# Performance work log

Measured on AMD Instinct MI355X. Metric: run time of the kernel, lower is better.

## Reference

```python
import jax, jax.numpy as jnp
import numpy as np

B, S, D = 4, 2048, 1024
H, DK, DV = 16, 64, 64  # heads, key_size, size_per_head
NEG = 1000000000.0


def setup_inputs() -> dict:
    key = jax.random.key(0)
    ks = jax.random.split(key, 8)
    scale = 1.0 / np.sqrt(D)
    return {
        "q": jax.random.normal(ks[0], (B, S, D), jnp.float32),
        "k": jax.random.normal(ks[1], (B, S, D), jnp.float32),
        "v": jax.random.normal(ks[2], (B, S, D), jnp.float32),
        "v_mask": jax.random.randint(ks[3], (B, S), 0, 2).astype(jnp.float32),
        "q_mask": jax.random.randint(ks[4], (B, S), 0, 2).astype(jnp.float32),
        "Wq": jax.random.normal(ks[5], (D, H * DK), jnp.float32) * scale,
        "Wk": jax.random.normal(ks[6], (D, H * DK), jnp.float32) * scale,
        "Wv": jax.random.normal(ks[7], (D, H * DV), jnp.float32) * scale,
    }


def reference(q, k, v, v_mask, q_mask, Wq, Wk, Wv):
    b, sq, _ = q.shape
    sk = k.shape[1]
    # projections + head split: [B, H, S, Dh]
    qw = (q @ Wq).reshape(b, sq, H, DK).transpose(0, 2, 1, 3)
    kw = (k @ Wk).reshape(b, sk, H, DK).transpose(0, 2, 1, 3)
    vw = (v @ Wv).reshape(b, sk, H, DV).transpose(0, 2, 1, 3)
    # scaled dot-product scores [B, H, Sq, Sk]
    a = jnp.einsum("bhqd,bhkd->bhqk", qw, kw) / jnp.sqrt(jnp.float32(DK))
    # additive kv-mask (v_mask over key axis)
    a = a - (1.0 - v_mask)[:, None, None, :] * NEG
    # causal (mask_right=True): subtract 1e9 on strictly-upper triangle
    causal = jnp.triu(jnp.ones((sq, sk), jnp.float32), k=1) * NEG
    a = a - causal[None, None]
    a = jax.nn.softmax(a, axis=-1)
    o = jnp.einsum("bhqk,bhkd->bhqd", a, vw)
    o = o.transpose(0, 2, 1, 3).reshape(b, sq, H * DV)
    # multiplicative query mask on output
    return o * q_mask[:, :, None]
```

## Files before the change

### kernel.cpp

```cpp
#include <hip/hip_runtime.h>

#define S_LEN 2048
#define NHEAD 16

typedef float f32x4 __attribute__((ext_vector_type(4)));
typedef __bf16 bf16x8 __attribute__((ext_vector_type(8)));
typedef __bf16 bf16x4 __attribute__((ext_vector_type(4)));

#define AS1 __attribute__((address_space(1)))
#define AS3 __attribute__((address_space(3)))

__device__ __forceinline__ void gl2lds16(const void* g, void* l) {
    __builtin_amdgcn_global_load_lds((const AS1 unsigned int*)g,
                                     (AS3 unsigned int*)l, 16, 0, 0);
}
__device__ __forceinline__ void wb_leave4() {
    asm volatile("s_waitcnt vmcnt(4)\n\ts_barrier" ::: "memory");
}
__device__ __forceinline__ void wb_drain() {
    asm volatile("s_waitcnt vmcnt(0)\n\ts_barrier" ::: "memory");
}

__global__ __launch_bounds__(256) void cast_swizzle_kernel(
    const float* __restrict__ q, const float* __restrict__ k,
    const float* __restrict__ v, __bf16* __restrict__ out)
{
    int gid = blockIdx.x * 256 + threadIdx.x;
    int z   = gid >> 20;
    int rem = gid & 1048575;
    int r   = rem >> 7;
    int c   = rem & 127;
    const float* src = (z == 0 ? q : z == 1 ? k : v) + (size_t)r * 1024 + c * 8;
    float4 a = *(const float4*)src;
    float4 b = *(const float4*)(src + 4);
    bf16x8 t;
    t[0] = (__bf16)a.x; t[1] = (__bf16)a.y; t[2] = (__bf16)a.z; t[3] = (__bf16)a.w;
    t[4] = (__bf16)b.x; t[5] = (__bf16)b.y; t[6] = (__bf16)b.z; t[7] = (__bf16)b.w;
    int cp = (c & ~7) | ((c ^ r) & 7);
    *(bf16x8*)(out + (size_t)z * 8388608 + (size_t)r * 1024 + cp * 8) = t;
}

__global__ __launch_bounds__(256) void transpose_cast_kernel(
    const float* __restrict__ W0, const float* __restrict__ W1,
    const float* __restrict__ W2, __bf16* __restrict__ Wt)
{
    int z = blockIdx.z;
    const float* W = (z == 0 ? W0 : z == 1 ? W1 : W2);
    __bf16* out = Wt + (size_t)z * 1048576;
    __shared__ float tile[32][33];
    int bx = blockIdx.x, by = blockIdx.y;
    int tid = threadIdx.x;
    int tx = tid & 31, ty = tid >> 5;
    for (int i = 0; i < 32; i += 8)
        tile[ty + i][tx] = W[(size_t)(by * 32 + ty + i) * 1024 + bx * 32 + tx];
    __syncthreads();
    if (tid < 128) {
        int nl = tid >> 2, kc = tid & 3;
        int n = bx * 32 + nl;
        int kbase = by * 32 + kc * 8;
        bf16x8 t;
        for (int j = 0; j < 8; j++) t[j] = (__bf16)tile[kc * 8 + j][nl];
        int cp = ((kbase >> 3) ^ n) & 7;
        *(bf16x8*)(out + (size_t)n * 1024 + (kbase & ~63) + cp * 8) = t;
    }
}

__global__ __launch_bounds__(256, 3) void proj_gemm_kernel(
    const __bf16* __restrict__ Abf, const __bf16* __restrict__ Wt,
    __bf16* __restrict__ qw, __bf16* __restrict__ kw, __bf16* __restrict__ vt)
{
    int z = blockIdx.z;
    const __bf16* A = Abf + (size_t)z * 8388608;
    const __bf16* B = Wt + (size_t)z * 1048576;
    __shared__ __align__(16) char smem[49152];

    int tid = threadIdx.x;
    int bm = blockIdx.x, bn = blockIdx.y;
    int wave = tid >> 6, lane = tid & 63;
    int wm = (wave >> 1) * 64, wn = (wave & 1) * 64;
    int lrow = lane & 15;
    int q4 = lane >> 4;
    int l4r = lane >> 2, j4 = lane & 3;

    auto pf = [&](int kb) {
        int sl = kb % 3;
        int k0 = kb * 32;
        int segbyte = (k0 >> 6) * 128;
        int cbase = (k0 & 32) >> 3;
        for (int i = 0; i < 2; i++) {
            int r = wave * 32 + i * 16 + l4r;
            int cl = j4 ^ ((r >> 1) & 3);
            int phys = ((cbase + cl) ^ r) & 7;
            gl2lds16((const char*)A + (size_t)(bm * 128 + r) * 2048 + segbyte + phys * 16,
                     smem + sl * 8192 + wave * 2048 + i * 1024);
            gl2lds16((const char*)B + (size_t)(bn * 128 + r) * 2048 + segbyte + phys * 16,
                     smem + 24576 + sl * 8192 + wave * 2048 + i * 1024);
        }
    };

    f32x4 zero = {0.f, 0.f, 0.f, 0.f};
    f32x4 acc[4][4];
    for (int mt = 0; mt < 4; mt++)
        for (int nt = 0; nt < 4; nt++) acc[mt][nt] = zero;

    pf(0); pf(1);
    __syncthreads();
    for (int kb = 0; kb < 32; kb++) {
        if (kb == 31) wb_drain(); else wb_leave4();
        if (kb + 2 < 32) pf(kb + 2);
        int sA = (kb % 3) * 8192, sB = 24576 + (kb % 3) * 8192;
        bf16x8 af[4], bfv[4];
        for (int mt = 0; mt < 4; mt++) {
            int r = wm + mt * 16 + lrow;
            af[mt] = *(const bf16x8*)(smem + sA + r * 64 + (q4 ^ ((r >> 1) & 3)) * 16);
        }
        for (int nt = 0; nt < 4; nt++) {
            int r = wn + nt * 16 + lrow;
            bfv[nt] = *(const bf16x8*)(smem + sB + r * 64 + (q4 ^ ((r >> 1) & 3)) * 16);
        }
        for (int mt = 0; mt < 4; mt++)
            for (int nt = 0; nt < 4; nt++)
                acc[mt][nt] = __builtin_amdgcn_mfma_f32_16x16x32_bf16(
                    af[mt], bfv[nt], acc[mt][nt], 0, 0, 0);
    }
    __syncthreads();
    __bf16* T = (__bf16*)smem;

    float oscale = (z == 0) ? 0.125f : 1.0f;
    int rowoff = q4 * 4;
    int b = bm >> 4;
    int s_base = (bm & 15) * 128;
    if (z < 2) {
        for (int mt = 0; mt < 4; mt++) {
            for (int nt = 0; nt < 4; nt++) {
                int n_local = wn + nt * 16 + lrow;
                int hl = n_local >> 6, d = n_local & 63;
                for (int reg = 0; reg < 4; reg++) {
                    int s_local = wm + mt * 16 + rowoff + reg;
                    int s = s_base + s_local;
                    int dp = (d & 7) | ((((d >> 3) ^ s) & 7) << 3);
                    T[s_local * 136 + hl * 64 + dp] = (__bf16)(acc[mt][nt][reg] * oscale);
                }
            }
        }
        __syncthreads();
        char* gq = (char*)(z == 0 ? qw : kw);
        for (int i = 0; i < 8; i++) {
            int id = tid + i * 256;
            int hl = id >> 10, r = (id >> 3) & 127, j = id & 7;
            float4 val = *(float4*)((char*)T + r * 272 + hl * 128 + j * 16);
            *(float4*)(gq + ((size_t)((b * 16 + bn * 2 + hl) * 2048) + s_base + r) * 128
                          + j * 16) = val;
        }
    } else {
        for (int mt = 0; mt < 4; mt++) {
            int s0 = wm + mt * 16 + rowoff;
            int seg = s0 >> 6, j0 = s0 & 63;
            for (int nt = 0; nt < 4; nt++) {
                int n_local = wn + nt * 16 + lrow;
                int d = n_local & 63;
                int hi = ((j0 >> 3) ^ d) & 7;
                bf16x4 pk;
                for (int reg = 0; reg < 4; reg++) pk[reg] = (__bf16)acc[mt][nt][reg];
                *(bf16x4*)&T[n_local * 136 + seg * 64 + hi * 8 + (j0 & 7)] = pk;
            }
        }
        __syncthreads();
        char* gv = (char*)vt;
        for (int i = 0; i < 8; i++) {
            int id = tid + i * 256;
            int nl = id >> 4, j = id & 15;
            int hl = nl >> 6, dv = nl & 63;
            float4 val = *(float4*)((char*)T + nl * 272 + j * 16);
            *(float4*)(gv + (((size_t)((b * 16 + bn * 2 + hl) * 64 + dv)) * 2048 + s_base) * 2
                          + j * 16) = val;
        }
    }
}

__global__ __launch_bounds__(256, 2) void attn_kernel(
    const __bf16* __restrict__ QW, const __bf16* __restrict__ KW,
    const __bf16* __restrict__ VT, const float* __restrict__ v_mask,
    const float* __restrict__ q_mask, float* __restrict__ out)
{
    int lin = blockIdx.x + (blockIdx.y << 4);
    int xcd = lin & 7;
    int jj  = lin >> 3;
    int bh  = (xcd << 3) + (jj >> 4);
    int bx  = jj & 15;
    int b = bh >> 4, h = bh & 15;

    __shared__ __align__(16) char lds[40960];
    char* Kb0 = lds;
    char* Vb0 = lds + 16384;
    char* Pw  = lds + 32768;

    int tid = threadIdx.x;
    int wave = tid >> 6, lane = tid & 63;
    int mloc = lane & 15, q4 = lane >> 4;
    int rowoff = q4 * 4, x7 = mloc & 7;
    char* Pme = Pw + wave * 2048;

    const char* Krow = (const char*)KW + (size_t)bh * 2048 * 128;
    const char* Vrow = (const char*)VT + (size_t)bh * 64 * 4096;
    const float* vmrow = v_mask + (size_t)b * 2048;

    int id0 = tid, id1 = tid + 256;

    auto stage = [&](int kb, int slot) {
        char* kd = Kb0 + slot * 8192;
        char* vd = Vb0 + slot * 8192;
        gl2lds16(Krow + (size_t)(kb * 64 + (id0 >> 3)) * 128 + (id0 & 7) * 16,
                 kd + id0 * 16);
        gl2lds16(Krow + (size_t)(kb * 64 + (id1 >> 3)) * 128 + (id1 & 7) * 16,
                 kd + id1 * 16);
        gl2lds16(Vrow + (size_t)(id0 >> 3) * 4096 + (size_t)kb * 128 + (id0 & 7) * 16,
                 vd + id0 * 16);
        gl2lds16(Vrow + (size_t)(id1 >> 3) * 4096 + (size_t)kb * 128 + (id1 & 7) * 16,
                 vd + id1 * 16);
    };

    f32x4 zero = {0.f, 0.f, 0.f, 0.f};

    for (int p = 0; p < 2; p++) {
        int qb = p ? (31 - bx) : bx;
        const char* Qrow = (const char*)QW +
                           ((size_t)bh * 2048 + qb * 64 + wave * 16) * 128;
        bf16x8 qfr[2];
        for (int kc = 0; kc < 2; kc++)
            qfr[kc] = *(const bf16x8*)(Qrow + mloc * 128 + (((kc * 4 + q4) ^ x7) << 4));

        stage(0, 0);
        float4 vm4[4];
        for (int m = 0; m < 4; m++)
            vm4[m] = *(const float4*)(vmrow + m * 16 + rowoff);

        f32x4 o_acc[4];
        for (int nt = 0; nt < 4; nt++) o_acc[nt] = zero;
        float lt = 0.f;

        for (int kb = 0; kb <= qb; kb++) {
            int slot = kb & 1;
            if (kb < qb) {
                stage(kb + 1, slot ^ 1);
                asm volatile("s_waitcnt vmcnt(8)\n\ts_barrier" ::: "memory");
            } else {
                asm volatile("s_waitcnt vmcnt(4)\n\ts_barrier" ::: "memory");
            }
            const char* Kls = Kb0 + slot * 8192;
            const char* Vls = Vb0 + slot * 8192;

            f32x4 sacc[4];
            for (int m = 0; m < 4; m++) sacc[m] = zero;
            for (int kc = 0; kc < 2; kc++) {
                bf16x8 kfr[4];
                for (int m = 0; m < 4; m++)
                    kfr[m] = *(const bf16x8*)(Kls + (m * 16 + mloc) * 128 +
                                              (((kc * 4 + q4) ^ x7) << 4));
                for (int m = 0; m < 4; m++)
                    sacc[m] = __builtin_amdgcn_mfma_f32_16x16x32_bf16(
                        kfr[m], qfr[kc], sacc[m], 0, 0, 0);
            }
            for (int m = 0; m < 4; m++) {
                float pen[4];
                pen[0] = fmaf(1.0f - vm4[m].x, 1.0e9f, 12.0f);
                pen[1] = fmaf(1.0f - vm4[m].y, 1.0e9f, 12.0f);
                pen[2] = fmaf(1.0f - vm4[m].z, 1.0e9f, 12.0f);
                pen[3] = fmaf(1.0f - vm4[m].w, 1.0e9f, 12.0f);
                float pv[4];
                for (int reg = 0; reg < 4; reg++)
                    pv[reg] = __expf(sacc[m][reg] - pen[reg]);
                if (kb == qb)
                    for (int reg = 0; reg < 4; reg++)
                        if (m * 16 + rowoff + reg > wave * 16 + mloc) pv[reg] = 0.f;
                lt += (pv[0] + pv[1]) + (pv[2] + pv[3]);
                bf16x4 pk;
                for (int reg = 0; reg < 4; reg++) pk[reg] = (__bf16)pv[reg];
                *(bf16x4*)(Pme + mloc * 128 +
                           (((m * 2 + (q4 >> 1)) ^ x7) << 4) + (q4 & 1) * 8) = pk;
            }
            if (kb < qb)
                for (int m = 0; m < 4; m++)
                    vm4[m] = *(const float4*)(vmrow + (kb + 1) * 64 + m * 16 + rowoff);
            for (int kc = 0; kc < 2; kc++) {
                bf16x8 afr = *(const bf16x8*)(Pme + mloc * 128 +
                                              (((kc * 4 + q4) ^ x7) << 4));
                bf16x8 vfr[4];
                for (int nt = 0; nt < 4; nt++)
                    vfr[nt] = *(const bf16x8*)(Vls + (nt * 16 + mloc) * 128 +
                                               (((kc * 4 + q4) ^ x7) << 4));
                for (int nt = 0; nt < 4; nt++)
                    o_acc[nt] = __builtin_amdgcn_mfma_f32_16x16x32_bf16(
                        afr, vfr[nt], o_acc[nt], 0, 0, 0);
            }
            asm volatile("s_barrier" ::: "memory");
        }

        lt += __shfl_xor(lt, 16);
        lt += __shfl_xor(lt, 32);

        if (__any(lt == 0.0f)) {
            float l2 = 0.f;
            bool degrow = (lt == 0.0f);
            int qrow = qb * 64 + wave * 16 + mloc;
            for (int kb2 = 0; kb2 < 32; kb2++) {
                bf16x8 vfr[4][2];
                for (int nt = 0; nt < 4; nt++)
                    for (int kc = 0; kc < 2; kc++)
                        vfr[nt][kc] = *(const bf16x8*)(Vrow +
                            (size_t)(nt * 16 + mloc) * 4096 +
                            kb2 * 128 + (((kc * 4 + q4) ^ x7) << 4));
                for (int kc = 0; kc < 2; kc++) {
                    const float* vmp = vmrow + kb2 * 64 + kc * 32 + q4 * 8;
                    float4 va = *(const float4*)vmp;
                    float4 vb4 = *(const float4*)(vmp + 4);
                    float vmj[8] = {va.x, va.y, va.z, va.w,
                                    vb4.x, vb4.y, vb4.z, vb4.w};
                    int kg0 = kb2 * 64 + kc * 32 + q4 * 8;
                    bf16x8 af;
                    float cnt = 0.f;
                    for (int j = 0; j < 8; j++) {
                        float ind = degrow ? ((kg0 + j <= qrow) ? 1.0f : vmj[j]) : 0.0f;
                        af[j] = (__bf16)ind;
                        cnt += ind;
                    }
                    l2 += cnt;
                    for (int nt = 0; nt < 4; nt++)
                        o_acc[nt] = __builtin_amdgcn_mfma_f32_16x16x32_bf16(
                            af, vfr[nt][kc], o_acc[nt], 0, 0, 0);
                }
            }
            l2 += __shfl_xor(l2, 16);
            l2 += __shfl_xor(l2, 32);
            if (degrow) lt = l2;
        }

        float sc[4];
        for (int reg = 0; reg < 4; reg++) {
            float lq = __shfl(lt, rowoff + reg);
            sc[reg] = q_mask[b * 2048 + qb * 64 + wave * 16 + rowoff + reg] / lq;
        }
        for (int nt = 0; nt < 4; nt++)
            for (int reg = 0; reg < 4; reg++)
                out[((size_t)(b * 2048 + qb * 64 + wave * 16 + rowoff + reg)) * 1024 +
                    h * 64 + nt * 16 + mloc] = o_acc[nt][reg] * sc[reg];
    }
}

extern "C" void kernel_launch(void* const* d_in, const int* in_sizes, int n_in,
                              void* d_out, int out_size, void* d_ws, size_t ws_size,
                              hipStream_t stream)
{
    const float* q      = (const float*)d_in[0];
    const float* k      = (const float*)d_in[1];
    const float* v      = (const float*)d_in[2];
    const float* v_mask = (const float*)d_in[3];
    const float* q_mask = (const float*)d_in[4];
    const float* Wq     = (const float*)d_in[5];
    const float* Wk     = (const float*)d_in[6];
    const float* Wv     = (const float*)d_in[7];
    float* out = (float*)d_out;

    __bf16* Abf = (__bf16*)d_ws;
    __bf16* Wt  = Abf + (size_t)3 * 8388608;
    __bf16* qw  = Wt + (size_t)3 * 1048576;
    __bf16* kw  = qw + (size_t)8388608;
    __bf16* vt  = kw + (size_t)8388608;

    cast_swizzle_kernel<<<12288, 256, 0, stream>>>(q, k, v, Abf);
    transpose_cast_kernel<<<dim3(32, 32, 3), 256, 0, stream>>>(Wq, Wk, Wv, Wt);
    proj_gemm_kernel<<<dim3(64, 8, 3), 256, 0, stream>>>(Abf, Wt, qw, kw, vt);
    attn_kernel<<<dim3(16, 64), 256, 0, stream>>>(qw, kw, vt, v_mask, q_mask, out);
}
```

Before: 308.5 us.

## Double query tile per block to 128 rows and stage v_mask in LDS

Each attention block now handles 128 query rows, with each wave owning two 16-row sub-tiles. Every K/V tile staged into LDS is therefore reused across twice as many queries, which halves K/V global traffic and barrier overhead per query. The v_mask row is preloaded once into LDS instead of being read from global memory every iteration. The grid halves to 512 blocks and LDS per block grows to 56KB, which may reduce occupancy, raise register pressure, and leave fewer blocks to balance the causal workload.

```diff
diff --git a/kernel.cpp b/kernel.cpp
--- a/kernel.cpp
+++ b/kernel.cpp
@@ -183,23 +183,22 @@
     const __bf16* __restrict__ VT, const float* __restrict__ v_mask,
     const float* __restrict__ q_mask, float* __restrict__ out)
 {
-    int lin = blockIdx.x + (blockIdx.y << 4);
+    int lin = blockIdx.x + (blockIdx.y << 3);
     int xcd = lin & 7;
     int jj  = lin >> 3;
-    int bh  = (xcd << 3) + (jj >> 4);
-    int bx  = jj & 15;
+    int bh  = (xcd << 3) + (jj >> 3);
+    int bx  = jj & 7;
     int b = bh >> 4, h = bh & 15;
 
-    __shared__ __align__(16) char lds[40960];
-    char* Kb0 = lds;
-    char* Vb0 = lds + 16384;
-    char* Pw  = lds + 32768;
+    __shared__ __align__(16) char lds[57344];
+    char*  Pw  = lds + 32768;
+    float* vms = (float*)(lds + 49152);
 
     int tid = threadIdx.x;
     int wave = tid >> 6, lane = tid & 63;
     int mloc = lane & 15, q4 = lane >> 4;
     int rowoff = q4 * 4, x7 = mloc & 7;
-    char* Pme = Pw + wave * 2048;
+    char* Pme = Pw + wave * 4096;
 
     const char* Krow = (const char*)KW + (size_t)bh * 2048 * 128;
     const char* Vrow = (const char*)VT + (size_t)bh * 64 * 4096;
@@ -208,8 +207,8 @@
     int id0 = tid, id1 = tid + 256;
 
     auto stage = [&](int kb, int slot) {
-        char* kd = Kb0 + slot * 8192;
-        char* vd = Vb0 + slot * 8192;
+        char* kd = lds + slot * 8192;
+        char* vd = lds + 16384 + slot * 8192;
         gl2lds16(Krow + (size_t)(kb * 64 + (id0 >> 3)) * 128 + (id0 & 7) * 16,
                  kd + id0 * 16);
         gl2lds16(Krow + (size_t)(kb * 64 + (id1 >> 3)) * 128 + (id1 & 7) * 16,
@@ -220,89 +219,109 @@
                  vd + id1 * 16);
     };
 
+    gl2lds16((const char*)vmrow + id0 * 16, (char*)vms + id0 * 16);
+    gl2lds16((const char*)vmrow + 4096 + id0 * 16, (char*)vms + 4096 + id0 * 16);
+
     f32x4 zero = {0.f, 0.f, 0.f, 0.f};
 
     for (int p = 0; p < 2; p++) {
-        int qb = p ? (31 - bx) : bx;
+        int g = p ? (15 - bx) : bx;
+        int jmax = 2 * g + 1;
         const char* Qrow = (const char*)QW +
-                           ((size_t)bh * 2048 + qb * 64 + wave * 16) * 128;
-        bf16x8 qfr[2];
-        for (int kc = 0; kc < 2; kc++)
-            qfr[kc] = *(const bf16x8*)(Qrow + mloc * 128 + (((kc * 4 + q4) ^ x7) << 4));
+                           ((size_t)bh * 2048 + g * 128 + wave * 32) * 128;
+        bf16x8 qfr[2][2];
+        for (int s = 0; s < 2; s++)
+            for (int kc = 0; kc < 2; kc++)
+                qfr[s][kc] = *(const bf16x8*)(Qrow + (s * 16 + mloc) * 128 +
+                                              (((kc * 4 + q4) ^ x7) << 4));
 
         stage(0, 0);
-        float4 vm4[4];
-        for (int m = 0; m < 4; m++)
-            vm4[m] = *(const float4*)(vmrow + m * 16 + rowoff);
-
-        f32x4 o_acc[4];
-        for (int nt = 0; nt < 4; nt++) o_acc[nt] = zero;
-        float lt = 0.f;
-
-        for (int kb = 0; kb <= qb; kb++) {
-            int slot = kb & 1;
-            if (kb < qb) {
-                stage(kb + 1, slot ^ 1);
-                asm volatile("s_waitcnt vmcnt(8)\n\ts_barrier" ::: "memory");
+
+        f32x4 o_acc[2][4];
+        for (int s = 0; s < 2; s++)
+            for (int nt = 0; nt < 4; nt++) o_acc[s][nt] = zero;
+        float lt[2] = {0.f, 0.f};
+
+        for (int j = 0; j <= jmax; j++) {
+            int slot = j & 1;
+            if (j < jmax) {
+                stage(j + 1, slot ^ 1);
+                asm volatile("s_waitcnt vmcnt(4)\n\ts_barrier" ::: "memory");
             } else {
-                asm volatile("s_waitcnt vmcnt(4)\n\ts_barrier" ::: "memory");
-            }
-            const char* Kls = Kb0 + slot * 8192;
-            const char* Vls = Vb0 + slot * 8192;
-
-            f32x4 sacc[4];
-            for (int m = 0; m < 4; m++) sacc[m] = zero;
+                asm volatile("s_waitcnt vmcnt(0)\n\ts_barrier" ::: "memory");
+            }
+            const char* Kls = lds + slot * 8192;
+            const char* Vls = lds + 16384 + slot * 8192;
+
+            f32x4 sacc[2][4];
+            for (int s = 0; s < 2; s++)
+                for (int m = 0; m < 4; m++) sacc[s][m] = zero;
             for (int kc = 0; kc < 2; kc++) {
                 bf16x8 kfr[4];
                 for (int m = 0; m < 4; m++)
                     kfr[m] = *(const bf16x8*)(Kls + (m * 16 + mloc) * 128 +
                                               (((kc * 4 + q4) ^ x7) << 4));
-                for (int m = 0; m < 4; m++)
-                    sacc[m] = __builtin_amdgcn_mfma_f32_16x16x32_bf16(
-                        kfr[m], qfr[kc], sacc[m], 0, 0, 0);
-            }
-            for (int m = 0; m < 4; m++) {
-                float pen[4];
-                pen[0] = fmaf(1.0f - vm4[m].x, 1.0e9f, 12.0f);
-                pen[1] = fmaf(1.0f - vm4[m].y, 1.0e9f, 12.0f);
-                pen[2] = fmaf(1.0f - vm4[m].z, 1.0e9f, 12.0f);
-                pen[3] = fmaf(1.0f - vm4[m].w, 1.0e9f, 12.0f);
-                float pv[4];
-                for (int reg = 0; reg < 4; reg++)
-                    pv[reg] = __expf(sacc[m][reg] - pen[reg]);
-                if (kb == qb)
+                for (int m = 0; m < 4; m++) {
+                    sacc[0][m] = __builtin_amdgcn_mfma_f32_16x16x32_bf16(
+                        kfr[m], qfr[0][kc], sacc[0][m], 0, 0, 0);
+                    sacc[1][m] = __builtin_amdgcn_mfma_f32_16x16x32_bf16(
+                        kfr[m], qfr[1][kc], sacc[1][m], 0, 0, 0);
+                }
+            }
+
+            for (int s = 0; s < 2; s++) {
+                int qrow = g * 128 + wave * 32 + s * 16 + mloc;
+                bool clip = (64 * j + 63 > g * 128 + wave * 32 + s * 16);
+                for (int m = 0; m < 4; m++) {
+                    float4 vm4 = *(const float4*)&vms[j * 64 + m * 16 + rowoff];
+                    float pen[4];
+                    pen[0] = fmaf(1.0f - vm4.x, 1.0e9f, 12.0f);
+                    pen[1] = fmaf(1.0f - vm4.y, 1.0e9f, 12.0f);
+                    pen[2] = fmaf(1.0f - vm4.z, 1.0e9f, 12.0f);
+                    pen[3] = fmaf(1.0f - vm4.w, 1.0e9f, 12.0f);
+                    float pv[4];
                     for (int reg = 0; reg < 4; reg++)
-                        if (m * 16 + rowoff + reg > wave * 16 + mloc) pv[reg] = 0.f;
-                lt += (pv[0] + pv[1]) + (pv[2] + pv[3]);
-                bf16x4 pk;
-                for (int reg = 0; reg < 4; reg++) pk[reg] = (__bf16)pv[reg];
-                *(bf16x4*)(Pme + mloc * 128 +
-                           (((m * 2 + (q4 >> 1)) ^ x7) << 4) + (q4 & 1) * 8) = pk;
-            }
-            if (kb < qb)
-                for (int m = 0; m < 4; m++)
-                    vm4[m] = *(const float4*)(vmrow + (kb + 1) * 64 + m * 16 + rowoff);
+                        pv[reg] = __expf(sacc[s][m][reg] - pen[reg]);
+                    if (clip) {
+                        int kb0 = 64 * j + m * 16 + rowoff;
+                        for (int reg = 0; reg < 4; reg++)
+                            if (kb0 + reg > qrow) pv[reg] = 0.f;
+                    }
+                    lt[s] += (pv[0] + pv[1]) + (pv[2] + pv[3]);
+                    bf16x4 pk;
+                    for (int reg = 0; reg < 4; reg++) pk[reg] = (__bf16)pv[reg];
+                    *(bf16x4*)(Pme + s * 2048 + mloc * 128 +
+                               (((m * 2 + (q4 >> 1)) ^ x7) << 4) + (q4 & 1) * 8) = pk;
+                }
+            }
+
             for (int kc = 0; kc < 2; kc++) {
-                bf16x8 afr = *(const bf16x8*)(Pme + mloc * 128 +
-                                              (((kc * 4 + q4) ^ x7) << 4));
+                bf16x8 afr0 = *(const bf16x8*)(Pme + mloc * 128 +
+                                               (((kc * 4 + q4) ^ x7) << 4));
+                bf16x8 afr1 = *(const bf16x8*)(Pme + 2048 + mloc * 128 +
+                                               (((kc * 4 + q4) ^ x7) << 4));
                 bf16x8 vfr[4];
                 for (int nt = 0; nt < 4; nt++)
                     vfr[nt] = *(const bf16x8*)(Vls + (nt * 16 + mloc) * 128 +
                                                (((kc * 4 + q4) ^ x7) << 4));
-                for (int nt = 0; nt < 4; nt++)
-                    o_acc[nt] = __builtin_amdgcn_mfma_f32_16x16x32_bf16(
-                        afr, vfr[nt], o_acc[nt], 0, 0, 0);
-            }
+                for (int nt = 0; nt < 4; nt++) {
+                    o_acc[0][nt] = __builtin_amdgcn_mfma_f32_16x16x32_bf16(
+                        afr0, vfr[nt], o_acc[0][nt], 0, 0, 0);
+                    o_acc[1][nt] = __builtin_amdgcn_mfma_f32_16x16x32_bf16(
+                        afr1, vfr[nt], o_acc[1][nt], 0, 0, 0);
+                }
+            }
+
             asm volatile("s_barrier" ::: "memory");
         }
 
-        lt += __shfl_xor(lt, 16);
-        lt += __shfl_xor(lt, 32);
-
-        if (__any(lt == 0.0f)) {
-            float l2 = 0.f;
-            bool degrow = (lt == 0.0f);
-            int qrow = qb * 64 + wave * 16 + mloc;
+        for (int s = 0; s < 2; s++) {
+            lt[s] += __shfl_xor(lt[s], 16);
+            lt[s] += __shfl_xor(lt[s], 32);
+        }
+
+        if (__any((lt[0] == 0.0f) || (lt[1] == 0.0f))) {
+            float l2[2] = {0.f, 0.f};
             for (int kb2 = 0; kb2 < 32; kb2++) {
                 bf16x8 vfr[4][2];
                 for (int nt = 0; nt < 4; nt++)
@@ -311,39 +330,51 @@
                             (size_t)(nt * 16 + mloc) * 4096 +
                             kb2 * 128 + (((kc * 4 + q4) ^ x7) << 4));
                 for (int kc = 0; kc < 2; kc++) {
-                    const float* vmp = vmrow + kb2 * 64 + kc * 32 + q4 * 8;
+                    const float* vmp = &vms[kb2 * 64 + kc * 32 + q4 * 8];
                     float4 va = *(const float4*)vmp;
                     float4 vb4 = *(const float4*)(vmp + 4);
                     float vmj[8] = {va.x, va.y, va.z, va.w,
                                     vb4.x, vb4.y, vb4.z, vb4.w};
                     int kg0 = kb2 * 64 + kc * 32 + q4 * 8;
-                    bf16x8 af;
-                    float cnt = 0.f;
-                    for (int j = 0; j < 8; j++) {
-                        float ind = degrow ? ((kg0 + j <= qrow) ? 1.0f : vmj[j]) : 0.0f;
-                        af[j] = (__bf16)ind;
-                        cnt += ind;
+                    for (int s = 0; s < 2; s++) {
+                        bool degrow = (lt[s] == 0.0f);
+                        int qrow = g * 128 + wave * 32 + s * 16 + mloc;
+                        bf16x8 af;
+                        float cnt = 0.f;
+                        for (int jx = 0; jx < 8; jx++) {
+                            float ind = degrow ? ((kg0 + jx <= qrow) ? 1.0f : vmj[jx])
+                                               : 0.0f;
+                            af[jx] = (__bf16)ind;
+                            cnt += ind;
+                        }
+                        l2[s] += cnt;
+                        for (int nt = 0; nt < 4; nt++)
+                            o_acc[s][nt] = __builtin_amdgcn_mfma_f32_16x16x32_bf16(
+                                af, vfr[nt][kc], o_acc[s][nt], 0, 0, 0);
                     }
-                    l2 += cnt;
-                    for (int nt = 0; nt < 4; nt++)
-                        o_acc[nt] = __builtin_amdgcn_mfma_f32_16x16x32_bf16(
-                            af, vfr[nt][kc], o_acc[nt], 0, 0, 0);
                 }
             }
-            l2 += __shfl_xor(l2, 16);
-            l2 += __shfl_xor(l2, 32);
-            if (degrow) lt = l2;
-        }
-
-        float sc[4];
-        for (int reg = 0; reg < 4; reg++) {
-            float lq = __shfl(lt, rowoff + reg);
-            sc[reg] = q_mask[b * 2048 + qb * 64 + wave * 16 + rowoff + reg] / lq;
-        }
-        for (int nt = 0; nt < 4; nt++)
-            for (int reg = 0; reg < 4; reg++)
-                out[((size_t)(b * 2048 + qb * 64 + wave * 16 + rowoff + reg)) * 1024 +
-                    h * 64 + nt * 16 + mloc] = o_acc[nt][reg] * sc[reg];
+            for (int s = 0; s < 2; s++) {
+                l2[s] += __shfl_xor(l2[s], 16);
+                l2[s] += __shfl_xor(l2[s], 32);
+                if (lt[s] == 0.0f) lt[s] = l2[s];
+            }
+        }
+
+        for (int s = 0; s < 2; s++) {
+            int q0 = g * 128 + wave * 32 + s * 16 + rowoff;
+            float sc[4];
+            for (int reg = 0; reg < 4; reg++) {
+                float lq = __shfl(lt[s], rowoff + reg);
+                sc[reg] = q_mask[b * 2048 + q0 + reg] / lq;
+            }
+            for (int nt = 0; nt < 4; nt++)
+                for (int reg = 0; reg < 4; reg++)
+                    out[((size_t)(b * 2048 + q0 + reg)) * 1024 +
+                        h * 64 + nt * 16 + mloc] = o_acc[s][nt][reg] * sc[reg];
+        }
+
+        asm volatile("s_waitcnt vmcnt(0) lgkmcnt(0)\n\ts_barrier" ::: "memory");
     }
 }
 
@@ -370,5 +401,5 @@
     cast_swizzle_kernel<<<12288, 256, 0, stream>>>(q, k, v, Abf);
     transpose_cast_kernel<<<dim3(32, 32, 3), 256, 0, stream>>>(Wq, Wk, Wv, Wt);
     proj_gemm_kernel<<<dim3(64, 8, 3), 256, 0, stream>>>(Abf, Wt, qw, kw, vt);
-    attn_kernel<<<dim3(16, 64), 256, 0, stream>>>(qw, kw, vt, v_mask, q_mask, out);
-}
+    attn_kernel<<<dim3(8, 64), 256, 0, stream>>>(qw, kw, vt, v_mask, q_mask, out);
+}
```

New measurement: 306.5 us. About the same (-0.7%).
